# Kernel tuning notes

Measured on AMD Instinct MI355X. Metric: run time of the kernel, lower is better.

The kernel has to match this reference:

```python
import jax, jax.numpy as jnp
import numpy as np

N_NODES = 50000


def _gcn_conv(x, W, b, src, dst, norm, n_nodes):
    # x: [N, Fin], W: [Fin, Fout]
    h = x @ W                                   # [N, Fout]
    msg = h[src] * norm[:, None]                # [E+N, Fout] edge messages
    out = jax.ops.segment_sum(msg, dst, num_segments=n_nodes)
    return out + b


def reference(x, edge_index, W1, b1, W2, b2):
    n = x.shape[0]
    # add self-loops (PyG GCNConv default add_self_loops=True)
    loop = jnp.arange(n, dtype=edge_index.dtype)
    src = jnp.concatenate([edge_index[0], loop])
    dst = jnp.concatenate([edge_index[1], loop])
    # symmetric degree normalization: deg over destination with unit weights
    deg = jax.ops.segment_sum(jnp.ones_like(dst, dtype=x.dtype), dst, num_segments=n)
    dinv = jnp.where(deg > 0, jax.lax.rsqrt(deg), 0.0)
    norm = dinv[src] * dinv[dst]                # [E+N]
    h = _gcn_conv(x, W1, b1, src, dst, norm, n)
    h = jax.nn.relu(h)
    out = _gcn_conv(h, W2, b2, src, dst, norm, n)
    return out


def setup_inputs() -> dict:
    key = jax.random.key(0)
    k1, k2, k3, k4 = jax.random.split(key, 4)
    n, e, fin, hid, fout = N_NODES, 800000, 128, 128, 64
    x = jax.random.normal(k1, (n, fin), dtype=jnp.float32)
    edge_index = jax.random.randint(k2, (2, e), 0, n, dtype=jnp.int64)
    # Glorot-ish init for linear weights, zero bias (PyG default)
    W1 = jax.random.normal(k3, (fin, hid), dtype=jnp.float32) / np.sqrt(fin)
    b1 = jnp.zeros((hid,), dtype=jnp.float32)
    W2 = jax.random.normal(k4, (hid, fout), dtype=jnp.float32) / np.sqrt(hid)
    b2 = jnp.zeros((fout,), dtype=jnp.float32)
    return {"x": x, "edge_index": edge_index, "W1": W1, "b1": b1, "W2": W2, "b2": b2}
```

## Files before the change

kernel.cpp:

```cpp
#include <hip/hip_runtime.h>
#include <hip/hip_bf16.h>


constexpr int FIN = 128;
constexpr int HID = 128;
constexpr int FOUT = 64;
constexpr int CAP = 48;
constexpr int NPB = 98;
constexpr int BCAP = 3072;
constexpr int OVF_MAX = 65536;

typedef __attribute__((ext_vector_type(8))) short s16x8;
typedef __attribute__((ext_vector_type(4))) float f32x4;

static __device__ __forceinline__ float bf2f(__hip_bfloat16 v) { return __bfloat162float(v); }
static __device__ __forceinline__ float lo2f(unsigned u) { union { unsigned i; float f; } c; c.i = u << 16; return c.f; }
static __device__ __forceinline__ float hi2f(unsigned u) { union { unsigned i; float f; } c; c.i = u & 0xffff0000u; return c.f; }
static __device__ __forceinline__ unsigned short f2bfu(float f) {
    __hip_bfloat16 h = __float2bfloat16(f);
    union { __hip_bfloat16 h; unsigned short u; } c; c.h = h; return c.u;
}
static __device__ __forceinline__ unsigned pack2(float a, float b) {
    return (unsigned)f2bfu(a) | ((unsigned)f2bfu(b) << 16);
}
static __device__ __forceinline__ void acc_add(float* acc, uint4 v) {
    acc[0] += lo2f(v.x); acc[1] += hi2f(v.x);
    acc[2] += lo2f(v.y); acc[3] += hi2f(v.y);
    acc[4] += lo2f(v.z); acc[5] += hi2f(v.z);
    acc[6] += lo2f(v.w); acc[7] += hi2f(v.w);
}

__global__ __launch_bounds__(256) void k_detect(const unsigned* __restrict__ xw,
                                                const int* __restrict__ eiw,
                                                int E, int* __restrict__ flags,
                                                int* __restrict__ gcur) {
    for (int i = threadIdx.x; i < 514; i += 256) gcur[i] = 0;
    __shared__ int s_bf16like, s_oddnz;
    if (threadIdx.x == 0) { s_bf16like = 0; s_oddnz = 0; }
    __syncthreads();
    int c = 0;
    for (int i = threadIdx.x; i < 4096; i += 256) {
        unsigned ex = ((xw[i] & 0xffffu) >> 7) & 0xffu;
        if (ex >= 117u && ex <= 130u) c++;
    }
    atomicAdd(&s_bf16like, c);
    int nz = 0;
    for (int i = threadIdx.x; i < 2048; i += 256)
        if (eiw[2 * i + 1] != 0) nz++;
    atomicAdd(&s_oddnz, nz);
    __syncthreads();
    if (threadIdx.x == 0) {
        flags[0] = (s_bf16like < 2048) ? 1 : 0;
        flags[1] = (s_oddnz == 0) ? 1 : 0;
    }
}

__global__ __launch_bounds__(256) void k_binA(const int* __restrict__ ei, int E, int N,
                                              int nbuk,
                                              int* __restrict__ gcur,
                                              int2* __restrict__ pairs,
                                              int2* __restrict__ ovfA,
                                              int* __restrict__ ovfAcnt,
                                              const int* __restrict__ flags) {
    __shared__ int hist[512];
    __shared__ int gbase[512];
    const int tid = threadIdx.x;
    const long base = (long)blockIdx.x * 2048;
    const bool i64 = flags[1] != 0;
    int se[8], de[8];
    for (int b = tid; b < nbuk; b += 256) hist[b] = 0;
    __syncthreads();
#pragma unroll
    for (int j = 0; j < 8; ++j) {
        long i = base + j * 256 + tid;
        int s = 0, d = -1;
        if (i < E) {
            if (i64) { s = ((const int2*)ei)[i].x; d = ((const int2*)(ei + 2 * (long)E))[i].x; }
            else     { s = ei[i]; d = ei[(long)E + i]; }
            if ((unsigned)s >= (unsigned)N || (unsigned)d >= (unsigned)N) d = -1;
        }
        se[j] = s; de[j] = d;
        if (d >= 0) atomicAdd(&hist[d / NPB], 1);
    }
    __syncthreads();
    for (int b = tid; b < nbuk; b += 256) {
        int h = hist[b];
        gbase[b] = h > 0 ? atomicAdd(&gcur[b], h) : 0;
        hist[b] = 0;
    }
    __syncthreads();
#pragma unroll
    for (int j = 0; j < 8; ++j) {
        int d = de[j];
        if (d < 0) continue;
        int b = d / NPB;
        int p = gbase[b] + atomicAdd(&hist[b], 1);
        if (p < BCAP) {
            pairs[(long)b * BCAP + p] = make_int2(d, se[j]);
        } else {
            int op = atomicAdd(ovfAcnt, 1);
            if (op < OVF_MAX) ovfA[op] = make_int2(d, se[j]);
        }
    }
}

__global__ __launch_bounds__(256) void k_binB(const int* __restrict__ gcur,
                                              const int2* __restrict__ pairs,
                                              int* __restrict__ cnt,
                                              int* __restrict__ slots,
                                              int2* __restrict__ ovf2,
                                              int* __restrict__ ovf2cnt, int N) {
    __shared__ int cntL[NPB];
    __shared__ __align__(16) int slotsL[NPB * CAP];
    const int b = blockIdx.x;
    const int tid = threadIdx.x;
    const int d0 = b * NPB;
    const int nd = min(NPB, N - d0);
    if (nd <= 0) return;
    for (int i = tid; i < NPB; i += 256) cntL[i] = 0;
    __syncthreads();
    const int c = min(gcur[b], BCAP);
    const int2* pb = pairs + (long)b * BCAP;
    for (int i = tid; i < c; i += 256) {
        int2 p = pb[i];
        int ld = p.x - d0;
        int pos = atomicAdd(&cntL[ld], 1);
        if (pos < CAP) {
            slotsL[ld * CAP + pos] = p.y;
        } else {
            int op = atomicAdd(ovf2cnt, 1);
            if (op < OVF_MAX) ovf2[op] = p;
        }
    }
    __syncthreads();
    for (int i = tid; i < nd; i += 256) cnt[d0 + i] = cntL[i];
    const uint4* sv = (const uint4*)slotsL;
    uint4* gv = (uint4*)(slots + (long)d0 * CAP);
    const int total4 = (nd * CAP) >> 2;
    for (int i = tid; i < total4; i += 256) gv[i] = sv[i];
}

__global__ __launch_bounds__(256) void k_patch(const int2* __restrict__ ovfA,
                                               const int* __restrict__ ovfAcnt,
                                               int* __restrict__ cnt,
                                               int* __restrict__ slots,
                                               int2* __restrict__ ovf2,
                                               int* __restrict__ ovf2cnt, int N) {
    int n = *ovfAcnt; n = n < OVF_MAX ? n : OVF_MAX;
    for (int i = blockIdx.x * 256 + threadIdx.x; i < n; i += gridDim.x * 256) {
        int2 p = ovfA[i];
        int pos = atomicAdd(&cnt[p.x], 1);
        if (pos < CAP) {
            slots[(long)p.x * CAP + pos] = p.y;
        } else {
            int op = atomicAdd(ovf2cnt, 1);
            if (op < OVF_MAX) ovf2[op] = p;
        }
    }
}

template<int CT>
__global__ __launch_bounds__(256) void k_gemm(const void* __restrict__ Xp, int x_follows_flag,
                                              const void* __restrict__ Wp,
                                              const int* __restrict__ cnt,
                                              __hip_bfloat16* __restrict__ G,
                                              const int* __restrict__ flags, int N) {
    constexpr int C = CT * 16;
    __shared__ __align__(16) short Wt[C * 136];
    const bool f32m = flags[0] != 0;
    const bool xf32 = (x_follows_flag != 0) && f32m;
    const int tid = threadIdx.x;
    for (int i = tid; i < 128 * C; i += 256) {
        int k = i / C, n = i % C;
        float wv = f32m ? ((const float*)Wp)[(long)k * C + n]
                        : bf2f(((const __hip_bfloat16*)Wp)[(long)k * C + n]);
        Wt[n * 136 + k] = (short)f2bfu(wv);
    }
    __syncthreads();
    const int w = tid >> 6, lane = tid & 63;
    const int m = lane & 15, quad = lane >> 4;
    const int rowA = blockIdx.x * 64 + w * 16 + m;
    const int rowc = rowA < N ? rowA : N - 1;
    s16x8 afr[4];
#pragma unroll
    for (int kc = 0; kc < 4; ++kc) {
        const int k0 = kc * 32 + quad * 8;
        if (!xf32) {
            afr[kc] = *(const s16x8*)((const __hip_bfloat16*)Xp + (long)rowc * 128 + k0);
        } else {
            const float* p = (const float*)Xp + (long)rowc * 128 + k0;
            s16x8 t;
#pragma unroll
            for (int j = 0; j < 8; ++j) t[j] = (short)f2bfu(p[j]);
            afr[kc] = t;
        }
    }
    const int rbase = blockIdx.x * 64 + w * 16 + quad * 4;
    float dv[4];
#pragma unroll
    for (int r = 0; r < 4; ++r) {
        int rr = min(rbase + r, N - 1);
        dv[r] = rsqrtf((float)(cnt[rr] + 1));
    }
#pragma unroll
    for (int ct = 0; ct < CT; ++ct) {
        f32x4 acc = {0.f, 0.f, 0.f, 0.f};
#pragma unroll
        for (int kc = 0; kc < 4; ++kc) {
            s16x8 bfr = *(const s16x8*)&Wt[(ct * 16 + m) * 136 + kc * 32 + quad * 8];
            acc = __builtin_amdgcn_mfma_f32_16x16x32_bf16(afr[kc], bfr, acc, 0, 0, 0);
        }
#pragma unroll
        for (int r = 0; r < 4; ++r) {
            int rr = rbase + r;
            if (rr < N) G[(long)rr * C + ct * 16 + m] = __float2bfloat16(dv[r] * acc[r]);
        }
    }
}

template<int F, int TILES, int LAYER1>
__global__ __launch_bounds__(256) void k_gather(const __hip_bfloat16* __restrict__ G,
                                                const int* __restrict__ cnt,
                                                const int* __restrict__ slots,
                                                const int2* __restrict__ ovf2,
                                                const int* __restrict__ ovf2cnt,
                                                const void* __restrict__ bias,
                                                void* __restrict__ outp,
                                                const int* __restrict__ flags, int N) {
    constexpr int SUBS = 8 / TILES;
    const int h = blockIdx.x & 7;
    const int nc = blockIdx.x >> 3;
    const int tile = h / SUBS;
    const int sub = h % SUBS;
    const int tid = threadIdx.x;
    const int grp = tid >> 2, lane = tid & 3;
    const int node = nc * (64 * SUBS) + sub * 64 + grp;
    if (node >= N) return;
    const int cd = cnt[node];
    const float wself = rsqrtf((float)(cd + 1));
    const int m = cd < CAP ? cd : CAP;
    const int* sl = slots + (long)node * CAP;
    const __hip_bfloat16* Gt = G + tile * 32;
    float acc[8] = {0, 0, 0, 0, 0, 0, 0, 0};
    acc_add(acc, ((const uint4*)(Gt + (long)node * F))[lane]);
    int i = 0;
    for (; i + 3 < m; i += 4) {
        int s0 = sl[i], s1 = sl[i + 1], s2 = sl[i + 2], s3 = sl[i + 3];
        uint4 v0 = ((const uint4*)(Gt + (long)s0 * F))[lane];
        uint4 v1 = ((const uint4*)(Gt + (long)s1 * F))[lane];
        uint4 v2 = ((const uint4*)(Gt + (long)s2 * F))[lane];
        uint4 v3 = ((const uint4*)(Gt + (long)s3 * F))[lane];
        acc_add(acc, v0); acc_add(acc, v1); acc_add(acc, v2); acc_add(acc, v3);
    }
    for (; i < m; ++i)
        acc_add(acc, ((const uint4*)(Gt + (long)sl[i] * F))[lane]);
    if (cd > CAP) {
        int oc = *ovf2cnt; oc = oc < OVF_MAX ? oc : OVF_MAX;
        for (int j = 0; j < oc; ++j)
            if (ovf2[j].x == node)
                acc_add(acc, ((const uint4*)(Gt + (long)ovf2[j].y * F))[lane]);
    }
    const bool f32m = flags[0] != 0;
    const int c0 = tile * 32 + lane * 8;
    float bv[8];
    if (f32m) {
        const float4* bp = (const float4*)((const float*)bias + c0);
        float4 b0 = bp[0], b1 = bp[1];
        bv[0] = b0.x; bv[1] = b0.y; bv[2] = b0.z; bv[3] = b0.w;
        bv[4] = b1.x; bv[5] = b1.y; bv[6] = b1.z; bv[7] = b1.w;
    } else {
        uint4 b = *(const uint4*)((const __hip_bfloat16*)bias + c0);
        bv[0] = lo2f(b.x); bv[1] = hi2f(b.x); bv[2] = lo2f(b.y); bv[3] = hi2f(b.y);
        bv[4] = lo2f(b.z); bv[5] = hi2f(b.z); bv[6] = lo2f(b.w); bv[7] = hi2f(b.w);
    }
    float o[8];
#pragma unroll
    for (int c = 0; c < 8; ++c) {
        float v = wself * acc[c] + bv[c];
        o[c] = (LAYER1 && v < 0.f) ? 0.f : v;
    }
    if (LAYER1 || !f32m) {
        uint4 pv = { pack2(o[0], o[1]), pack2(o[2], o[3]), pack2(o[4], o[5]), pack2(o[6], o[7]) };
        ((uint4*)outp)[(long)node * (F / 8) + tile * 4 + lane] = pv;
    } else {
        float4* op = (float4*)((float*)outp + (long)node * F + c0);
        op[0] = make_float4(o[0], o[1], o[2], o[3]);
        op[1] = make_float4(o[4], o[5], o[6], o[7]);
    }
}

extern "C" void kernel_launch(void* const* d_in, const int* in_sizes, int n_in,
                              void* d_out, int out_size, void* d_ws, size_t ws_size,
                              hipStream_t stream) {
    const void* x  = d_in[0];
    const int*  ei = (const int*)d_in[1];
    const void* W1 = d_in[2];
    const void* b1 = d_in[3];
    const void* W2 = d_in[4];
    const void* b2 = d_in[5];

    const int N = in_sizes[0] / FIN;
    const int E = in_sizes[1] / 2;
    const int nbuk = (N + NPB - 1) / NPB;

    char* ws = (char*)d_ws;
    int*   flags   = (int*)ws;
    int*   gcur    = (int*)(ws + 4096);
    int*   ovfAcnt = gcur + 512;
    int*   ovf2cnt = gcur + 513;
    int*   cnt     = (int*)(ws + 65536);
    int2*  ovfA    = (int2*)(ws + 524288);
    int2*  ovf2    = (int2*)(ws + 1048576);
    int*   slots   = (int*)(ws + 2097152);
    __hip_bfloat16* g  = (__hip_bfloat16*)(ws + 11730944);
    __hip_bfloat16* g2 = g;
    int2*  pairs   = (int2*)(ws + 24530944);
    __hip_bfloat16* h1 = (__hip_bfloat16*)(ws + 24530944);

    const int GB = (N + 63) / 64;
    const int AB = (E + 2047) / 2048;

    k_detect<<<1, 256, 0, stream>>>((const unsigned*)x, ei, E, flags, gcur);
    k_binA<<<AB, 256, 0, stream>>>(ei, E, N, nbuk, gcur, pairs, ovfA, ovfAcnt, flags);
    k_binB<<<nbuk, 256, 0, stream>>>(gcur, pairs, cnt, slots, ovf2, ovf2cnt, N);
    k_patch<<<32, 256, 0, stream>>>(ovfA, ovfAcnt, cnt, slots, ovf2, ovf2cnt, N);
    k_gemm<8><<<GB, 256, 0, stream>>>(x, 1, W1, cnt, g, flags, N);
    k_gather<128, 4, 1><<<((N + 127) / 128) * 8, 256, 0, stream>>>(g, cnt, slots, ovf2, ovf2cnt, b1, h1, flags, N);
    k_gemm<4><<<GB, 256, 0, stream>>>(h1, 0, W2, cnt, g2, flags, N);
    k_gather<64, 2, 0><<<((N + 255) / 256) * 8, 256, 0, stream>>>(g2, cnt, slots, ovf2, ovf2cnt, b2, d_out, flags, N);
}
```

Measured before the change: 233.9 us.

## Pack edge bins and adjacency slots into 16-bit indices, gather full rows per node

Edge bin pairs are packed into one 32-bit word (local dst in the high 16 bits, src in the low 16), and the per-node adjacency slots become 16-bit when N fits, halving the index traffic in binning and gather. The gather kernels now let each node group cover the full feature row instead of splitting columns across eight block slices, and the gather loop is unrolled to eight loads. A fallback path handles large N through a direct atomic CSR build, with cnt zeroing moved into the detect kernel. This adds register pressure from the deeper unroll, and the path choice hinges on N limits.

```diff
diff --git a/kernel.cpp b/kernel.cpp
--- a/kernel.cpp
+++ b/kernel.cpp
@@ -33,7 +33,11 @@
 __global__ __launch_bounds__(256) void k_detect(const unsigned* __restrict__ xw,
                                                 const int* __restrict__ eiw,
                                                 int E, int* __restrict__ flags,
-                                                int* __restrict__ gcur) {
+                                                int* __restrict__ gcur,
+                                                int* __restrict__ cnt, int N) {
+    for (long i = (long)blockIdx.x * 256 + threadIdx.x; i < N; i += (long)gridDim.x * 256)
+        cnt[i] = 0;
+    if (blockIdx.x != 0) return;
     for (int i = threadIdx.x; i < 514; i += 256) gcur[i] = 0;
     __shared__ int s_bf16like, s_oddnz;
     if (threadIdx.x == 0) { s_bf16like = 0; s_oddnz = 0; }
@@ -58,7 +62,7 @@
 __global__ __launch_bounds__(256) void k_binA(const int* __restrict__ ei, int E, int N,
                                               int nbuk,
                                               int* __restrict__ gcur,
-                                              int2* __restrict__ pairs,
+                                              unsigned* __restrict__ pairs,
                                               int2* __restrict__ ovfA,
                                               int* __restrict__ ovfAcnt,
                                               const int* __restrict__ flags) {
@@ -96,7 +100,7 @@
         int b = d / NPB;
         int p = gbase[b] + atomicAdd(&hist[b], 1);
         if (p < BCAP) {
-            pairs[(long)b * BCAP + p] = make_int2(d, se[j]);
+            pairs[(long)b * BCAP + p] = ((unsigned)(d - b * NPB) << 16) | (unsigned)se[j];
         } else {
             int op = atomicAdd(ovfAcnt, 1);
             if (op < OVF_MAX) ovfA[op] = make_int2(d, se[j]);
@@ -105,13 +109,13 @@
 }
 
 __global__ __launch_bounds__(256) void k_binB(const int* __restrict__ gcur,
-                                              const int2* __restrict__ pairs,
+                                              const unsigned* __restrict__ pairs,
                                               int* __restrict__ cnt,
-                                              int* __restrict__ slots,
+                                              unsigned short* __restrict__ slots,
                                               int2* __restrict__ ovf2,
                                               int* __restrict__ ovf2cnt, int N) {
     __shared__ int cntL[NPB];
-    __shared__ __align__(16) int slotsL[NPB * CAP];
+    __shared__ __align__(16) unsigned short slotsL[NPB * CAP];
     const int b = blockIdx.x;
     const int tid = threadIdx.x;
     const int d0 = b * NPB;
@@ -120,30 +124,31 @@
     for (int i = tid; i < NPB; i += 256) cntL[i] = 0;
     __syncthreads();
     const int c = min(gcur[b], BCAP);
-    const int2* pb = pairs + (long)b * BCAP;
+    const unsigned* pb = pairs + (long)b * BCAP;
     for (int i = tid; i < c; i += 256) {
-        int2 p = pb[i];
-        int ld = p.x - d0;
+        unsigned p = pb[i];
+        int ld = p >> 16;
         int pos = atomicAdd(&cntL[ld], 1);
         if (pos < CAP) {
-            slotsL[ld * CAP + pos] = p.y;
+            slotsL[ld * CAP + pos] = (unsigned short)(p & 0xffffu);
         } else {
             int op = atomicAdd(ovf2cnt, 1);
-            if (op < OVF_MAX) ovf2[op] = p;
+            if (op < OVF_MAX) ovf2[op] = make_int2(d0 + ld, (int)(p & 0xffffu));
         }
     }
     __syncthreads();
     for (int i = tid; i < nd; i += 256) cnt[d0 + i] = cntL[i];
     const uint4* sv = (const uint4*)slotsL;
     uint4* gv = (uint4*)(slots + (long)d0 * CAP);
-    const int total4 = (nd * CAP) >> 2;
-    for (int i = tid; i < total4; i += 256) gv[i] = sv[i];
-}
-
+    const int total8 = (nd * CAP) >> 3;
+    for (int i = tid; i < total8; i += 256) gv[i] = sv[i];
+}
+
+template<typename ST>
 __global__ __launch_bounds__(256) void k_patch(const int2* __restrict__ ovfA,
                                                const int* __restrict__ ovfAcnt,
                                                int* __restrict__ cnt,
-                                               int* __restrict__ slots,
+                                               ST* __restrict__ slots,
                                                int2* __restrict__ ovf2,
                                                int* __restrict__ ovf2cnt, int N) {
     int n = *ovfAcnt; n = n < OVF_MAX ? n : OVF_MAX;
@@ -151,11 +156,32 @@
         int2 p = ovfA[i];
         int pos = atomicAdd(&cnt[p.x], 1);
         if (pos < CAP) {
-            slots[(long)p.x * CAP + pos] = p.y;
+            slots[(long)p.x * CAP + pos] = (ST)p.y;
         } else {
             int op = atomicAdd(ovf2cnt, 1);
             if (op < OVF_MAX) ovf2[op] = p;
         }
+    }
+}
+
+__global__ __launch_bounds__(256) void k_build_direct(const int* __restrict__ ei, int E, int N,
+                                                      int* __restrict__ cnt,
+                                                      int* __restrict__ slots,
+                                                      int2* __restrict__ ovf2,
+                                                      int* __restrict__ ovf2cnt,
+                                                      const int* __restrict__ flags) {
+    long i = (long)blockIdx.x * 256 + threadIdx.x;
+    if (i >= E) return;
+    int s, d;
+    if (flags[1]) { s = ((const int2*)ei)[i].x; d = ((const int2*)(ei + 2 * (long)E))[i].x; }
+    else          { s = ei[i]; d = ei[(long)E + i]; }
+    if ((unsigned)s >= (unsigned)N || (unsigned)d >= (unsigned)N) return;
+    int pos = atomicAdd(&cnt[d], 1);
+    if (pos < CAP) {
+        slots[(long)d * CAP + pos] = s;
+    } else {
+        int op = atomicAdd(ovf2cnt, 1);
+        if (op < OVF_MAX) ovf2[op] = make_int2(d, s);
     }
 }
 
@@ -218,50 +244,60 @@
     }
 }
 
-template<int F, int TILES, int LAYER1>
+template<int F, int LAYER1, typename ST>
 __global__ __launch_bounds__(256) void k_gather(const __hip_bfloat16* __restrict__ G,
                                                 const int* __restrict__ cnt,
-                                                const int* __restrict__ slots,
+                                                const ST* __restrict__ slots,
                                                 const int2* __restrict__ ovf2,
                                                 const int* __restrict__ ovf2cnt,
                                                 const void* __restrict__ bias,
                                                 void* __restrict__ outp,
                                                 const int* __restrict__ flags, int N) {
-    constexpr int SUBS = 8 / TILES;
-    const int h = blockIdx.x & 7;
-    const int nc = blockIdx.x >> 3;
-    const int tile = h / SUBS;
-    const int sub = h % SUBS;
+    constexpr int L = F / 8;
+    constexpr int NODES = 256 / L;
     const int tid = threadIdx.x;
-    const int grp = tid >> 2, lane = tid & 3;
-    const int node = nc * (64 * SUBS) + sub * 64 + grp;
+    const int grp = tid / L, lane = tid % L;
+    const int node = blockIdx.x * NODES + grp;
     if (node >= N) return;
     const int cd = cnt[node];
     const float wself = rsqrtf((float)(cd + 1));
     const int m = cd < CAP ? cd : CAP;
-    const int* sl = slots + (long)node * CAP;
-    const __hip_bfloat16* Gt = G + tile * 32;
+    const ST* sl = slots + (long)node * CAP;
     float acc[8] = {0, 0, 0, 0, 0, 0, 0, 0};
-    acc_add(acc, ((const uint4*)(Gt + (long)node * F))[lane]);
+    acc_add(acc, ((const uint4*)(G + (long)node * F))[lane]);
     int i = 0;
+    for (; i + 7 < m; i += 8) {
+        int s0 = sl[i], s1 = sl[i + 1], s2 = sl[i + 2], s3 = sl[i + 3];
+        int s4 = sl[i + 4], s5 = sl[i + 5], s6 = sl[i + 6], s7 = sl[i + 7];
+        uint4 v0 = ((const uint4*)(G + (long)s0 * F))[lane];
+        uint4 v1 = ((const uint4*)(G + (long)s1 * F))[lane];
+        uint4 v2 = ((const uint4*)(G + (long)s2 * F))[lane];
+        uint4 v3 = ((const uint4*)(G + (long)s3 * F))[lane];
+        uint4 v4 = ((const uint4*)(G + (long)s4 * F))[lane];
+        uint4 v5 = ((const uint4*)(G + (long)s5 * F))[lane];
+        uint4 v6 = ((const uint4*)(G + (long)s6 * F))[lane];
+        uint4 v7 = ((const uint4*)(G + (long)s7 * F))[lane];
+        acc_add(acc, v0); acc_add(acc, v1); acc_add(acc, v2); acc_add(acc, v3);
+        acc_add(acc, v4); acc_add(acc, v5); acc_add(acc, v6); acc_add(acc, v7);
+    }
     for (; i + 3 < m; i += 4) {
         int s0 = sl[i], s1 = sl[i + 1], s2 = sl[i + 2], s3 = sl[i + 3];
-        uint4 v0 = ((const uint4*)(Gt + (long)s0 * F))[lane];
-        uint4 v1 = ((const uint4*)(Gt + (long)s1 * F))[lane];
-        uint4 v2 = ((const uint4*)(Gt + (long)s2 * F))[lane];
-        uint4 v3 = ((const uint4*)(Gt + (long)s3 * F))[lane];
+        uint4 v0 = ((const uint4*)(G + (long)s0 * F))[lane];
+        uint4 v1 = ((const uint4*)(G + (long)s1 * F))[lane];
+        uint4 v2 = ((const uint4*)(G + (long)s2 * F))[lane];
+        uint4 v3 = ((const uint4*)(G + (long)s3 * F))[lane];
         acc_add(acc, v0); acc_add(acc, v1); acc_add(acc, v2); acc_add(acc, v3);
     }
     for (; i < m; ++i)
-        acc_add(acc, ((const uint4*)(Gt + (long)sl[i] * F))[lane]);
+        acc_add(acc, ((const uint4*)(G + (long)sl[i] * F))[lane]);
     if (cd > CAP) {
         int oc = *ovf2cnt; oc = oc < OVF_MAX ? oc : OVF_MAX;
         for (int j = 0; j < oc; ++j)
             if (ovf2[j].x == node)
-                acc_add(acc, ((const uint4*)(Gt + (long)ovf2[j].y * F))[lane]);
+                acc_add(acc, ((const uint4*)(G + (long)ovf2[j].y * F))[lane]);
     }
     const bool f32m = flags[0] != 0;
-    const int c0 = tile * 32 + lane * 8;
+    const int c0 = lane * 8;
     float bv[8];
     if (f32m) {
         const float4* bp = (const float4*)((const float*)bias + c0);
@@ -281,7 +317,7 @@
     }
     if (LAYER1 || !f32m) {
         uint4 pv = { pack2(o[0], o[1]), pack2(o[2], o[3]), pack2(o[4], o[5]), pack2(o[6], o[7]) };
-        ((uint4*)outp)[(long)node * (F / 8) + tile * 4 + lane] = pv;
+        ((uint4*)outp)[(long)node * L + lane] = pv;
     } else {
         float4* op = (float4*)((float*)outp + (long)node * F + c0);
         op[0] = make_float4(o[0], o[1], o[2], o[3]);
@@ -311,21 +347,36 @@
     int*   cnt     = (int*)(ws + 65536);
     int2*  ovfA    = (int2*)(ws + 524288);
     int2*  ovf2    = (int2*)(ws + 1048576);
-    int*   slots   = (int*)(ws + 2097152);
+    unsigned short* slots16 = (unsigned short*)(ws + 2097152);
+    int*   slots32 = (int*)(ws + 2097152);
     __hip_bfloat16* g  = (__hip_bfloat16*)(ws + 11730944);
     __hip_bfloat16* g2 = g;
-    int2*  pairs   = (int2*)(ws + 24530944);
+    unsigned* pairs = (unsigned*)(ws + 24530944);
     __hip_bfloat16* h1 = (__hip_bfloat16*)(ws + 24530944);
 
     const int GB = (N + 63) / 64;
     const int AB = (E + 2047) / 2048;
-
-    k_detect<<<1, 256, 0, stream>>>((const unsigned*)x, ei, E, flags, gcur);
-    k_binA<<<AB, 256, 0, stream>>>(ei, E, N, nbuk, gcur, pairs, ovfA, ovfAcnt, flags);
-    k_binB<<<nbuk, 256, 0, stream>>>(gcur, pairs, cnt, slots, ovf2, ovf2cnt, N);
-    k_patch<<<32, 256, 0, stream>>>(ovfA, ovfAcnt, cnt, slots, ovf2, ovf2cnt, N);
-    k_gemm<8><<<GB, 256, 0, stream>>>(x, 1, W1, cnt, g, flags, N);
-    k_gather<128, 4, 1><<<((N + 127) / 128) * 8, 256, 0, stream>>>(g, cnt, slots, ovf2, ovf2cnt, b1, h1, flags, N);
-    k_gemm<4><<<GB, 256, 0, stream>>>(h1, 0, W2, cnt, g2, flags, N);
-    k_gather<64, 2, 0><<<((N + 255) / 256) * 8, 256, 0, stream>>>(g2, cnt, slots, ovf2, ovf2cnt, b2, d_out, flags, N);
-}
+    const int EB = (E + 255) / 256;
+
+    k_detect<<<64, 256, 0, stream>>>((const unsigned*)x, ei, E, flags, gcur, cnt, N);
+
+    if (N <= 65536 && nbuk <= 512) {
+        k_binA<<<AB, 256, 0, stream>>>(ei, E, N, nbuk, gcur, pairs, ovfA, ovfAcnt, flags);
+        k_binB<<<nbuk, 256, 0, stream>>>(gcur, pairs, cnt, slots16, ovf2, ovf2cnt, N);
+        k_patch<unsigned short><<<32, 256, 0, stream>>>(ovfA, ovfAcnt, cnt, slots16, ovf2, ovf2cnt, N);
+        k_gemm<8><<<GB, 256, 0, stream>>>(x, 1, W1, cnt, g, flags, N);
+        k_gather<128, 1, unsigned short><<<(N + 15) / 16, 256, 0, stream>>>(
+            g, cnt, slots16, ovf2, ovf2cnt, b1, h1, flags, N);
+        k_gemm<4><<<GB, 256, 0, stream>>>(h1, 0, W2, cnt, g2, flags, N);
+        k_gather<64, 0, unsigned short><<<(N + 31) / 32, 256, 0, stream>>>(
+            g2, cnt, slots16, ovf2, ovf2cnt, b2, d_out, flags, N);
+    } else {
+        k_build_direct<<<EB, 256, 0, stream>>>(ei, E, N, cnt, slots32, ovf2, ovf2cnt, flags);
+        k_gemm<8><<<GB, 256, 0, stream>>>(x, 1, W1, cnt, g, flags, N);
+        k_gather<128, 1, int><<<(N + 15) / 16, 256, 0, stream>>>(
+            g, cnt, slots32, ovf2, ovf2cnt, b1, h1, flags, N);
+        k_gemm<4><<<GB, 256, 0, stream>>>(h1, 0, W2, cnt, g2, flags, N);
+        k_gather<64, 0, int><<<(N + 31) / 32, 256, 0, stream>>>(
+            g2, cnt, slots32, ovf2, ovf2cnt, b2, d_out, flags, N);
+    }
+}
```

New measurement: 208.7 us. 10.8% less time.
